# Kernel tuning notes

Hardware: AMD Instinct MI355X
Metric: run time of the kernel (lower is better)

## Reference

```python
import jax, jax.numpy as jnp
import numpy as np

CHANNEL = 8
K_DIM = 16
D = CHANNEL * K_DIM
ROUT_IT = 3
TAU = 1.0
EPS = 1e-12  # torch F.normalize default


def _normalize(v):
    # L2 normalize over last dim, matching torch.nn.functional.normalize
    nrm = jnp.sqrt(jnp.sum(v * v, axis=-1, keepdims=True))
    return v / jnp.maximum(nrm, EPS)


def setup_inputs() -> dict:
    key = jax.random.key(0)
    k1, k2, k3, k4 = jax.random.split(key, 4)
    n, m = 50000, 32
    in_dim = D  # in_caps * k_dim = 8*16
    x = jax.random.normal(k1, (n, in_dim), dtype=jnp.float32)
    stdv = 1.0 / np.sqrt(float(in_dim))
    W = jax.random.uniform(k2, (D, in_dim), dtype=jnp.float32, minval=-stdv, maxval=stdv)
    b = jax.random.uniform(k3, (D,), dtype=jnp.float32, minval=-stdv, maxval=stdv)
    neighbor_id = jax.random.randint(k4, (n * m,), 0, n + 1, dtype=jnp.int64)
    return {"x": x, "W": W, "b": b, "neighbor_id": neighbor_id}


def reference(x, W, b, neighbor_id):
    n = x.shape[0]
    m = neighbor_id.shape[0] // n
    # fc + relu
    x = jax.nn.relu(x @ W.T + b)
    # per-capsule normalize
    x = _normalize(x.reshape(n, CHANNEL, K_DIM)).reshape(n, D)
    # append zero row for padded neighbor ids, gather neighbors
    z = jnp.concatenate([x, jnp.zeros((1, D), dtype=x.dtype)], axis=0)
    neighbors = z[neighbor_id].reshape(n, m, CHANNEL, K_DIM)
    x_caps = x.reshape(n, CHANNEL, K_DIM)
    u = x_caps
    for it in range(ROUT_IT):
        # agreement logits per (node, neighbor, channel)
        p = jnp.einsum('nck,nmck->nmc', u, neighbors)
        p = jax.nn.softmax(p / TAU, axis=-1)  # softmax over channels
        u = jnp.einsum('nmc,nmck->nck', p, neighbors) + x_caps
        if it < ROUT_IT - 1:
            u = _normalize(u)
    return u.reshape(n, D)
```

## Files before the change

kernel.cpp:

```cpp
#include <hip/hip_runtime.h>
#include <math.h>

#define CHANNEL 8
#define KDIM 16
#define DFULL 128
#define MNBR 32
#define ROUT_IT 3
#define TM1 64
#define NBS 20
#define SLP 20

typedef __attribute__((ext_vector_type(4))) float f32x4;
typedef __attribute__((ext_vector_type(8))) short short8;
typedef __attribute__((ext_vector_type(8))) _Float16 half8;
typedef __attribute__((ext_vector_type(2))) _Float16 half2v;

__device__ inline unsigned pk16(float a, float b) {
  auto r = __builtin_amdgcn_cvt_pkrtz(a, b);
  return __builtin_bit_cast(unsigned, r);
}
__device__ inline float fdot2(unsigned a, unsigned b, float c) {
  return __builtin_amdgcn_fdot2(__builtin_bit_cast(half2v, a),
                                __builtin_bit_cast(half2v, b), c, false);
}
__device__ inline float h2f_bits(ushort s) {
  union { ushort u; _Float16 h; } v; v.u = s; return (float)v.h;
}
template <int C>
__device__ inline float dppadd(float x) {
  int m = __builtin_amdgcn_update_dpp(0, __builtin_bit_cast(int, x), C, 0xF, 0xF, true);
  return x + __builtin_bit_cast(float, m);
}
__device__ inline float dppswap1(float x) {
  int m = __builtin_amdgcn_update_dpp(0, __builtin_bit_cast(int, x), 0xB1, 0xF, 0xF, true);
  return __builtin_bit_cast(float, m);
}

union H8 { unsigned u[4]; short8 v; };
__device__ inline short8 pack8h(float4 a, float4 b) {
  H8 r;
  r.u[0] = pk16(a.x, a.y); r.u[1] = pk16(a.z, a.w);
  r.u[2] = pk16(b.x, b.y); r.u[3] = pk16(b.z, b.w);
  return r.v;
}

__global__ __launch_bounds__(256) void wpack_kernel(const float* __restrict__ W,
                                                    ushort* __restrict__ wpk) {
  int task = blockIdx.x * 256 + threadIdx.x;
  if (task >= 2048) return;
  int f = task >> 6, l = task & 63;
  int kk = f >> 3, j = f & 7, L = l & 15, H = l >> 4;
  const float* src = W + (size_t)(j * 16 + L) * 128 + kk * 32 + H * 8;
  float4 a = *(const float4*)src;
  float4 b = *(const float4*)(src + 4);
  *(short8*)(wpk + (size_t)task * 8) = pack8h(a, b);
}

__global__ __launch_bounds__(256) void fc_mfma_kernel(
    const float* __restrict__ x, const ushort* __restrict__ wpk,
    const float* __restrict__ bias, ushort* __restrict__ z16, int n) {
  __shared__ __align__(16) float smem[TM1 * 132];

  const int t = threadIdx.x, lane = t & 63, w = t >> 6;

  {
    const uint4* gw = (const uint4*)wpk;
    uint4* lw = (uint4*)smem;
#pragma unroll
    for (int i = 0; i < 8; ++i) lw[i * 256 + t] = gw[i * 256 + t];
  }

  const int L = lane & 15, H = lane >> 4;
  const int r0 = blockIdx.x * TM1;
  const int row = r0 + w * 16 + L;
  const bool ok = row < n;
  const float4 z4 = make_float4(0.f, 0.f, 0.f, 0.f);

  const float* xr = x + (size_t)row * DFULL + H * 8;
  short8 af[4];
#pragma unroll
  for (int kk = 0; kk < 4; ++kk) {
    float4 xa = ok ? *(const float4*)(xr + kk * 32) : z4;
    float4 xb = ok ? *(const float4*)(xr + kk * 32 + 4) : z4;
    af[kk] = pack8h(xa, xb);
  }

  f32x4 acc[8];
#pragma unroll
  for (int j = 0; j < 8; ++j) {
    float bv = bias[j * 16 + L];
    acc[j] = (f32x4){bv, bv, bv, bv};
  }
  __syncthreads();
  const short8* wf = (const short8*)smem;
#pragma unroll
  for (int j = 0; j < 8; ++j)
#pragma unroll
    for (int kk = 0; kk < 4; ++kk) {
      short8 bfr = wf[(kk * 8 + j) * 64 + lane];
      acc[j] = __builtin_amdgcn_mfma_f32_16x16x32_f16(
          __builtin_bit_cast(half8, af[kk]), __builtin_bit_cast(half8, bfr),
          acc[j], 0, 0, 0);
    }
  __syncthreads();

  float* ys = smem;
  const int lr = w * 16 + H * 4;
#pragma unroll
  for (int j = 0; j < 8; ++j)
#pragma unroll
    for (int r = 0; r < 4; ++r)
      ys[(lr + r) * 132 + j * 16 + L] = fmaxf(acc[j][r], 0.f);
  __syncthreads();

#pragma unroll
  for (int pass = 0; pass < 2; ++pass) {
    int task = t + pass * 256;
    int rr = task >> 3, cc = task & 7;
    const float4* yr = (const float4*)(ys + rr * 132 + cc * 16);
    float4 a = yr[0], b = yr[1], c4 = yr[2], d4 = yr[3];
    float ss = a.x * a.x;
    ss = fmaf(a.y, a.y, ss); ss = fmaf(a.z, a.z, ss); ss = fmaf(a.w, a.w, ss);
    ss = fmaf(b.x, b.x, ss); ss = fmaf(b.y, b.y, ss); ss = fmaf(b.z, b.z, ss);
    ss = fmaf(b.w, b.w, ss); ss = fmaf(c4.x, c4.x, ss); ss = fmaf(c4.y, c4.y, ss);
    ss = fmaf(c4.z, c4.z, ss); ss = fmaf(c4.w, c4.w, ss); ss = fmaf(d4.x, d4.x, ss);
    ss = fmaf(d4.y, d4.y, ss); ss = fmaf(d4.z, d4.z, ss); ss = fmaf(d4.w, d4.w, ss);
    float sc = 1.f / fmaxf(sqrtf(ss), 1e-12f);
    int grow = r0 + rr;
    if (grow < n) {
      uint4 o0, o1;
      o0.x = pk16(a.x * sc, a.y * sc);  o0.y = pk16(a.z * sc, a.w * sc);
      o0.z = pk16(b.x * sc, b.y * sc);  o0.w = pk16(b.z * sc, b.w * sc);
      o1.x = pk16(c4.x * sc, c4.y * sc); o1.y = pk16(c4.z * sc, c4.w * sc);
      o1.z = pk16(d4.x * sc, d4.y * sc); o1.w = pk16(d4.z * sc, d4.w * sc);
      uint4* dst = (uint4*)(z16 + (size_t)grow * DFULL + cc * 16);
      dst[0] = o0; dst[1] = o1;
    } else if (grow == n) {
      uint4 zz = {0u, 0u, 0u, 0u};
      uint4* dst = (uint4*)(z16 + (size_t)grow * DFULL + cc * 16);
      dst[0] = zz; dst[1] = zz;
    }
  }
}

__global__ __launch_bounds__(256) void routing_kernel(
    const ushort* __restrict__ z16, const int* __restrict__ nid,
    float* __restrict__ out, int n) {
  __shared__ __align__(16) unsigned nbT[2][DFULL * NBS];
  __shared__ __align__(16) unsigned slpk[2][CHANNEL * SLP];
  __shared__ __align__(16) unsigned ulpk[2][64];

  const int t = threadIdx.x;
  const int h = t >> 7, g = t & 127;
  const int node = 2 * blockIdx.x + h;
  const int p = g >> 3, c = g & 7;
  const int d = g, uc = g >> 4;

  int2 rp = *(const int2*)(nid + node * MNBR + 2 * p);
  const uint4* s0 = (const uint4*)(z16 + (size_t)rp.x * DFULL + c * KDIM);
  const uint4* s1 = (const uint4*)(z16 + (size_t)rp.y * DFULL + c * KDIM);
  uint4 Ra = s0[0], Rb = s0[1];
  uint4 Sa = s1[0], Sb = s1[1];

  unsigned aw[8] = {Ra.x, Ra.y, Ra.z, Ra.w, Rb.x, Rb.y, Rb.z, Rb.w};
  unsigned bw[8] = {Sa.x, Sa.y, Sa.z, Sa.w, Sb.x, Sb.y, Sb.z, Sb.w};
  {
    unsigned* nb = nbT[h];
    const int pc = (p + 4 * c) & 15;
#pragma unroll
    for (int i = 0; i < 8; ++i) {
      unsigned ev = __builtin_amdgcn_perm(bw[i], aw[i], 0x05040100u);
      unsigned od = __builtin_amdgcn_perm(bw[i], aw[i], 0x07060302u);
      nb[(c * KDIM + 2 * i) * NBS + pc] = ev;
      nb[(c * KDIM + 2 * i + 1) * NBS + pc] = od;
    }
  }
  unsigned xdw = *((const unsigned*)(z16 + (size_t)node * DFULL) + (d >> 1));
  const float xk = (d & 1) ? h2f_bits((ushort)(xdw >> 16))
                           : h2f_bits((ushort)(xdw & 0xffffu));
  if (!(d & 1)) ulpk[h][d >> 1] = xdw;
  __syncthreads();

  const unsigned* nr = nbT[h] + d * NBS;
  const uint4 n0 = *(const uint4*)(nr + 0);
  const uint4 n1 = *(const uint4*)(nr + 4);
  const uint4 n2 = *(const uint4*)(nr + 8);
  const uint4 n3 = *(const uint4*)(nr + 12);
  const uint4* sq0 = (const uint4*)(slpk[h] + uc * SLP + 4 * ((0 - uc) & 3));
  const uint4* sq1 = (const uint4*)(slpk[h] + uc * SLP + 4 * ((1 - uc) & 3));
  const uint4* sq2 = (const uint4*)(slpk[h] + uc * SLP + 4 * ((2 - uc) & 3));
  const uint4* sq3 = (const uint4*)(slpk[h] + uc * SLP + 4 * ((3 - uc) & 3));
  const uint4* up = (const uint4*)(ulpk[h] + c * 8);

  for (int it = 0; it < ROUT_IT; ++it) {
    {
      uint4 u0 = up[0], u1 = up[1];
      float A0 = 0.f, A1 = 0.f;
      A0 = fdot2(aw[0], u0.x, A0); A1 = fdot2(bw[0], u0.x, A1);
      A0 = fdot2(aw[1], u0.y, A0); A1 = fdot2(bw[1], u0.y, A1);
      A0 = fdot2(aw[2], u0.z, A0); A1 = fdot2(bw[2], u0.z, A1);
      A0 = fdot2(aw[3], u0.w, A0); A1 = fdot2(bw[3], u0.w, A1);
      A0 = fdot2(aw[4], u1.x, A0); A1 = fdot2(bw[4], u1.x, A1);
      A0 = fdot2(aw[5], u1.y, A0); A1 = fdot2(bw[5], u1.y, A1);
      A0 = fdot2(aw[6], u1.z, A0); A1 = fdot2(bw[6], u1.z, A1);
      A0 = fdot2(aw[7], u1.w, A0); A1 = fdot2(bw[7], u1.w, A1);
      float e0 = __expf(A0), e1 = __expf(A1);
      float d0 = dppadd<0xB1>(e0);  float d1 = dppadd<0xB1>(e1);
      d0 = dppadd<0x4E>(d0);        d1 = dppadd<0x4E>(d1);
      d0 = dppadd<0x141>(d0);       d1 = dppadd<0x141>(d1);
      float ir0 = __builtin_amdgcn_rcpf(d0);
      float ir1 = __builtin_amdgcn_rcpf(d1);
      slpk[h][c * SLP + p] = pk16(e0 * ir0, e1 * ir1);
    }
    __syncthreads();
    {
      uint4 v0 = *sq0, v1 = *sq1, v2 = *sq2, v3 = *sq3;
      float A0 = xk, A1 = 0.f;
      A0 = fdot2(n0.x, v0.x, A0); A1 = fdot2(n2.x, v2.x, A1);
      A0 = fdot2(n0.y, v0.y, A0); A1 = fdot2(n2.y, v2.y, A1);
      A0 = fdot2(n0.z, v0.z, A0); A1 = fdot2(n2.z, v2.z, A1);
      A0 = fdot2(n0.w, v0.w, A0); A1 = fdot2(n2.w, v2.w, A1);
      A0 = fdot2(n1.x, v1.x, A0); A1 = fdot2(n3.x, v3.x, A1);
      A0 = fdot2(n1.y, v1.y, A0); A1 = fdot2(n3.y, v3.y, A1);
      A0 = fdot2(n1.z, v1.z, A0); A1 = fdot2(n3.z, v3.z, A1);
      A0 = fdot2(n1.w, v1.w, A0); A1 = fdot2(n3.w, v3.w, A1);
      float u = A0 + A1;
      if (it == ROUT_IT - 1) {
        out[(size_t)node * DFULL + d] = u;
      } else {
        float ssq = u * u;
        ssq = dppadd<0xB1>(ssq);
        ssq = dppadd<0x4E>(ssq);
        ssq = dppadd<0x141>(ssq);
        ssq = dppadd<0x140>(ssq);
        float sc = 1.f / fmaxf(sqrtf(ssq), 1e-12f);
        float un = u * sc;
        float uo = dppswap1(un);
        if (!(d & 1)) ulpk[h][d >> 1] = pk16(un, uo);
      }
    }
    __syncthreads();
  }
}

extern "C" void kernel_launch(void* const* d_in, const int* in_sizes, int n_in,
                              void* d_out, int out_size, void* d_ws, size_t ws_size,
                              hipStream_t stream) {
  const float* x = (const float*)d_in[0];
  const float* W = (const float*)d_in[1];
  const float* b = (const float*)d_in[2];
  const int* nid = (const int*)d_in[3];
  float* out = (float*)d_out;

  int n = in_sizes[0] / DFULL;
  int g1 = (n + 1 + TM1 - 1) / TM1;
  size_t zrows = (size_t)g1 * TM1;

  ushort* z16 = (ushort*)d_ws;
  ushort* wpk = (ushort*)d_ws + zrows * DFULL;

  wpack_kernel<<<8, 256, 0, stream>>>(W, wpk);
  fc_mfma_kernel<<<g1, 256, 0, stream>>>(x, wpk, b, z16, n);
  routing_kernel<<<n / 2, 256, 0, stream>>>(z16, nid, out, n);
}
```

Before: 150.1 us.

## Map one node per wavefront in routing kernel, replacing barriers with LDS waits

```diff
diff --git a/kernel.cpp b/kernel.cpp
--- a/kernel.cpp
+++ b/kernel.cpp
@@ -8,7 +8,6 @@
 #define ROUT_IT 3
 #define TM1 64
 #define NBS 20
-#define SLP 20
 
 typedef __attribute__((ext_vector_type(4))) float f32x4;
 typedef __attribute__((ext_vector_type(8))) short short8;
@@ -23,8 +22,11 @@
   return __builtin_amdgcn_fdot2(__builtin_bit_cast(half2v, a),
                                 __builtin_bit_cast(half2v, b), c, false);
 }
-__device__ inline float h2f_bits(ushort s) {
-  union { ushort u; _Float16 h; } v; v.u = s; return (float)v.h;
+__device__ inline float h2f_lo(unsigned w) {
+  union { ushort u; _Float16 h; } v; v.u = (ushort)(w & 0xffffu); return (float)v.h;
+}
+__device__ inline float h2f_hi(unsigned w) {
+  union { ushort u; _Float16 h; } v; v.u = (ushort)(w >> 16); return (float)v.h;
 }
 template <int C>
 __device__ inline float dppadd(float x) {
@@ -143,103 +145,162 @@
   }
 }
 
-__global__ __launch_bounds__(256) void routing_kernel(
+__global__ __launch_bounds__(128, 3) void routing_kernel(
     const ushort* __restrict__ z16, const int* __restrict__ nid,
     float* __restrict__ out, int n) {
   __shared__ __align__(16) unsigned nbT[2][DFULL * NBS];
-  __shared__ __align__(16) unsigned slpk[2][CHANNEL * SLP];
-  __shared__ __align__(16) unsigned ulpk[2][64];
+  __shared__ __align__(16) unsigned slT[2][CHANNEL * NBS];
+  __shared__ __align__(16) unsigned ulk[2][64];
 
   const int t = threadIdx.x;
-  const int h = t >> 7, g = t & 127;
-  const int node = 2 * blockIdx.x + h;
-  const int p = g >> 3, c = g & 7;
-  const int d = g, uc = g >> 4;
-
-  int2 rp = *(const int2*)(nid + node * MNBR + 2 * p);
-  const uint4* s0 = (const uint4*)(z16 + (size_t)rp.x * DFULL + c * KDIM);
-  const uint4* s1 = (const uint4*)(z16 + (size_t)rp.y * DFULL + c * KDIM);
-  uint4 Ra = s0[0], Rb = s0[1];
-  uint4 Sa = s1[0], Sb = s1[1];
-
-  unsigned aw[8] = {Ra.x, Ra.y, Ra.z, Ra.w, Rb.x, Rb.y, Rb.z, Rb.w};
-  unsigned bw[8] = {Sa.x, Sa.y, Sa.z, Sa.w, Sb.x, Sb.y, Sb.z, Sb.w};
+  const int wv = t >> 6, lane = t & 63;
+  const int node = blockIdx.x * 2 + wv;
+  const int q = lane >> 3, c = lane & 7;
+  const int cu = lane >> 4;
+
+  int4 ids = *(const int4*)(nid + node * MNBR + 4 * q);
+  const uint4* g0 = (const uint4*)(z16 + (size_t)ids.x * DFULL + c * KDIM);
+  const uint4* g1 = (const uint4*)(z16 + (size_t)ids.y * DFULL + c * KDIM);
+  const uint4* g2 = (const uint4*)(z16 + (size_t)ids.z * DFULL + c * KDIM);
+  const uint4* g3 = (const uint4*)(z16 + (size_t)ids.w * DFULL + c * KDIM);
+  uint4 R0a = g0[0], R0b = g0[1];
+  uint4 R1a = g1[0], R1b = g1[1];
+  uint4 R2a = g2[0], R2b = g2[1];
+  uint4 R3a = g3[0], R3b = g3[1];
+
+  const unsigned* zdw = (const unsigned*)z16;
+  ulk[wv][lane] = zdw[(size_t)node * 64 + lane];
+  unsigned xw0 = zdw[(size_t)node * 64 + (lane >> 1)];
+  unsigned xw1 = zdw[(size_t)node * 64 + 32 + (lane >> 1)];
+  const float xk0 = (lane & 1) ? h2f_hi(xw0) : h2f_lo(xw0);
+  const float xk1 = (lane & 1) ? h2f_hi(xw1) : h2f_lo(xw1);
+
+  unsigned r0[8] = {R0a.x, R0a.y, R0a.z, R0a.w, R0b.x, R0b.y, R0b.z, R0b.w};
+  unsigned r1[8] = {R1a.x, R1a.y, R1a.z, R1a.w, R1b.x, R1b.y, R1b.z, R1b.w};
+  unsigned r2[8] = {R2a.x, R2a.y, R2a.z, R2a.w, R2b.x, R2b.y, R2b.z, R2b.w};
+  unsigned r3[8] = {R3a.x, R3a.y, R3a.z, R3a.w, R3b.x, R3b.y, R3b.z, R3b.w};
+
   {
-    unsigned* nb = nbT[h];
-    const int pc = (p + 4 * c) & 15;
+    unsigned* nb = nbT[wv];
+    const int sl0 = (2 * q + 4 * c) & 15;
+    const int sl1 = (2 * q + 1 + 4 * c) & 15;
 #pragma unroll
     for (int i = 0; i < 8; ++i) {
-      unsigned ev = __builtin_amdgcn_perm(bw[i], aw[i], 0x05040100u);
-      unsigned od = __builtin_amdgcn_perm(bw[i], aw[i], 0x07060302u);
-      nb[(c * KDIM + 2 * i) * NBS + pc] = ev;
-      nb[(c * KDIM + 2 * i + 1) * NBS + pc] = od;
-    }
-  }
-  unsigned xdw = *((const unsigned*)(z16 + (size_t)node * DFULL) + (d >> 1));
-  const float xk = (d & 1) ? h2f_bits((ushort)(xdw >> 16))
-                           : h2f_bits((ushort)(xdw & 0xffffu));
-  if (!(d & 1)) ulpk[h][d >> 1] = xdw;
-  __syncthreads();
-
-  const unsigned* nr = nbT[h] + d * NBS;
-  const uint4 n0 = *(const uint4*)(nr + 0);
-  const uint4 n1 = *(const uint4*)(nr + 4);
-  const uint4 n2 = *(const uint4*)(nr + 8);
-  const uint4 n3 = *(const uint4*)(nr + 12);
-  const uint4* sq0 = (const uint4*)(slpk[h] + uc * SLP + 4 * ((0 - uc) & 3));
-  const uint4* sq1 = (const uint4*)(slpk[h] + uc * SLP + 4 * ((1 - uc) & 3));
-  const uint4* sq2 = (const uint4*)(slpk[h] + uc * SLP + 4 * ((2 - uc) & 3));
-  const uint4* sq3 = (const uint4*)(slpk[h] + uc * SLP + 4 * ((3 - uc) & 3));
-  const uint4* up = (const uint4*)(ulpk[h] + c * 8);
-
+      unsigned ev0 = __builtin_amdgcn_perm(r1[i], r0[i], 0x05040100u);
+      unsigned od0 = __builtin_amdgcn_perm(r1[i], r0[i], 0x07060302u);
+      unsigned ev1 = __builtin_amdgcn_perm(r3[i], r2[i], 0x05040100u);
+      unsigned od1 = __builtin_amdgcn_perm(r3[i], r2[i], 0x07060302u);
+      nb[(c * KDIM + 2 * i) * NBS + sl0] = ev0;
+      nb[(c * KDIM + 2 * i + 1) * NBS + sl0] = od0;
+      nb[(c * KDIM + 2 * i) * NBS + sl1] = ev1;
+      nb[(c * KDIM + 2 * i + 1) * NBS + sl1] = od1;
+    }
+  }
+  asm volatile("s_waitcnt lgkmcnt(0)" ::: "memory");
+
+  const unsigned* colA = nbT[wv] + lane * NBS;
+  const unsigned* colB = nbT[wv] + (lane + 64) * NBS;
+  const uint4 nA0 = *(const uint4*)(colA + 0);
+  const uint4 nA1 = *(const uint4*)(colA + 4);
+  const uint4 nA2 = *(const uint4*)(colA + 8);
+  const uint4 nA3 = *(const uint4*)(colA + 12);
+  const uint4 nB0 = *(const uint4*)(colB + 0);
+  const uint4 nB1 = *(const uint4*)(colB + 4);
+  const uint4 nB2 = *(const uint4*)(colB + 8);
+  const uint4 nB3 = *(const uint4*)(colB + 12);
+
+  const uint4* upk = (const uint4*)(ulk[wv] + c * 8);
+  const int o0 = 4 * ((0 - cu) & 3), o1 = 4 * ((1 - cu) & 3),
+            o2 = 4 * ((2 - cu) & 3), o3 = 4 * ((3 - cu) & 3);
+  const unsigned* sA = slT[wv] + cu * NBS;
+  const unsigned* sB = slT[wv] + (cu + 4) * NBS;
+  uint2* swr = (uint2*)(slT[wv]) + c * (NBS / 2) + q;
+
+#pragma unroll
   for (int it = 0; it < ROUT_IT; ++it) {
     {
-      uint4 u0 = up[0], u1 = up[1];
-      float A0 = 0.f, A1 = 0.f;
-      A0 = fdot2(aw[0], u0.x, A0); A1 = fdot2(bw[0], u0.x, A1);
-      A0 = fdot2(aw[1], u0.y, A0); A1 = fdot2(bw[1], u0.y, A1);
-      A0 = fdot2(aw[2], u0.z, A0); A1 = fdot2(bw[2], u0.z, A1);
-      A0 = fdot2(aw[3], u0.w, A0); A1 = fdot2(bw[3], u0.w, A1);
-      A0 = fdot2(aw[4], u1.x, A0); A1 = fdot2(bw[4], u1.x, A1);
-      A0 = fdot2(aw[5], u1.y, A0); A1 = fdot2(bw[5], u1.y, A1);
-      A0 = fdot2(aw[6], u1.z, A0); A1 = fdot2(bw[6], u1.z, A1);
-      A0 = fdot2(aw[7], u1.w, A0); A1 = fdot2(bw[7], u1.w, A1);
-      float e0 = __expf(A0), e1 = __expf(A1);
-      float d0 = dppadd<0xB1>(e0);  float d1 = dppadd<0xB1>(e1);
-      d0 = dppadd<0x4E>(d0);        d1 = dppadd<0x4E>(d1);
-      d0 = dppadd<0x141>(d0);       d1 = dppadd<0x141>(d1);
-      float ir0 = __builtin_amdgcn_rcpf(d0);
-      float ir1 = __builtin_amdgcn_rcpf(d1);
-      slpk[h][c * SLP + p] = pk16(e0 * ir0, e1 * ir1);
-    }
-    __syncthreads();
+      uint4 ua = upk[0], ub = upk[1];
+      float A0 = 0.f, A1 = 0.f, A2 = 0.f, A3 = 0.f;
+      A0 = fdot2(r0[0], ua.x, A0); A1 = fdot2(r1[0], ua.x, A1);
+      A2 = fdot2(r2[0], ua.x, A2); A3 = fdot2(r3[0], ua.x, A3);
+      A0 = fdot2(r0[1], ua.y, A0); A1 = fdot2(r1[1], ua.y, A1);
+      A2 = fdot2(r2[1], ua.y, A2); A3 = fdot2(r3[1], ua.y, A3);
+      A0 = fdot2(r0[2], ua.z, A0); A1 = fdot2(r1[2], ua.z, A1);
+      A2 = fdot2(r2[2], ua.z, A2); A3 = fdot2(r3[2], ua.z, A3);
+      A0 = fdot2(r0[3], ua.w, A0); A1 = fdot2(r1[3], ua.w, A1);
+      A2 = fdot2(r2[3], ua.w, A2); A3 = fdot2(r3[3], ua.w, A3);
+      A0 = fdot2(r0[4], ub.x, A0); A1 = fdot2(r1[4], ub.x, A1);
+      A2 = fdot2(r2[4], ub.x, A2); A3 = fdot2(r3[4], ub.x, A3);
+      A0 = fdot2(r0[5], ub.y, A0); A1 = fdot2(r1[5], ub.y, A1);
+      A2 = fdot2(r2[5], ub.y, A2); A3 = fdot2(r3[5], ub.y, A3);
+      A0 = fdot2(r0[6], ub.z, A0); A1 = fdot2(r1[6], ub.z, A1);
+      A2 = fdot2(r2[6], ub.z, A2); A3 = fdot2(r3[6], ub.z, A3);
+      A0 = fdot2(r0[7], ub.w, A0); A1 = fdot2(r1[7], ub.w, A1);
+      A2 = fdot2(r2[7], ub.w, A2); A3 = fdot2(r3[7], ub.w, A3);
+      float e0 = __expf(A0), e1 = __expf(A1), e2 = __expf(A2), e3 = __expf(A3);
+      float D0 = dppadd<0x141>(dppadd<0x4E>(dppadd<0xB1>(e0)));
+      float D1 = dppadd<0x141>(dppadd<0x4E>(dppadd<0xB1>(e1)));
+      float D2 = dppadd<0x141>(dppadd<0x4E>(dppadd<0xB1>(e2)));
+      float D3 = dppadd<0x141>(dppadd<0x4E>(dppadd<0xB1>(e3)));
+      float s0 = e0 * __builtin_amdgcn_rcpf(D0);
+      float s1 = e1 * __builtin_amdgcn_rcpf(D1);
+      float s2 = e2 * __builtin_amdgcn_rcpf(D2);
+      float s3 = e3 * __builtin_amdgcn_rcpf(D3);
+      uint2 sw; sw.x = pk16(s0, s1); sw.y = pk16(s2, s3);
+      *swr = sw;
+    }
+    asm volatile("s_waitcnt lgkmcnt(0)" ::: "memory");
     {
-      uint4 v0 = *sq0, v1 = *sq1, v2 = *sq2, v3 = *sq3;
-      float A0 = xk, A1 = 0.f;
-      A0 = fdot2(n0.x, v0.x, A0); A1 = fdot2(n2.x, v2.x, A1);
-      A0 = fdot2(n0.y, v0.y, A0); A1 = fdot2(n2.y, v2.y, A1);
-      A0 = fdot2(n0.z, v0.z, A0); A1 = fdot2(n2.z, v2.z, A1);
-      A0 = fdot2(n0.w, v0.w, A0); A1 = fdot2(n2.w, v2.w, A1);
-      A0 = fdot2(n1.x, v1.x, A0); A1 = fdot2(n3.x, v3.x, A1);
-      A0 = fdot2(n1.y, v1.y, A0); A1 = fdot2(n3.y, v3.y, A1);
-      A0 = fdot2(n1.z, v1.z, A0); A1 = fdot2(n3.z, v3.z, A1);
-      A0 = fdot2(n1.w, v1.w, A0); A1 = fdot2(n3.w, v3.w, A1);
-      float u = A0 + A1;
+      uint4 v;
+      float a = xk0, b = 0.f;
+      v = *(const uint4*)(sA + o0);
+      a = fdot2(nA0.x, v.x, a); b = fdot2(nA0.y, v.y, b);
+      a = fdot2(nA0.z, v.z, a); b = fdot2(nA0.w, v.w, b);
+      v = *(const uint4*)(sA + o1);
+      a = fdot2(nA1.x, v.x, a); b = fdot2(nA1.y, v.y, b);
+      a = fdot2(nA1.z, v.z, a); b = fdot2(nA1.w, v.w, b);
+      v = *(const uint4*)(sA + o2);
+      a = fdot2(nA2.x, v.x, a); b = fdot2(nA2.y, v.y, b);
+      a = fdot2(nA2.z, v.z, a); b = fdot2(nA2.w, v.w, b);
+      v = *(const uint4*)(sA + o3);
+      a = fdot2(nA3.x, v.x, a); b = fdot2(nA3.y, v.y, b);
+      a = fdot2(nA3.z, v.z, a); b = fdot2(nA3.w, v.w, b);
+      float u0 = a + b;
+      float e = xk1, f = 0.f;
+      v = *(const uint4*)(sB + o0);
+      e = fdot2(nB0.x, v.x, e); f = fdot2(nB0.y, v.y, f);
+      e = fdot2(nB0.z, v.z, e); f = fdot2(nB0.w, v.w, f);
+      v = *(const uint4*)(sB + o1);
+      e = fdot2(nB1.x, v.x, e); f = fdot2(nB1.y, v.y, f);
+      e = fdot2(nB1.z, v.z, e); f = fdot2(nB1.w, v.w, f);
+      v = *(const uint4*)(sB + o2);
+      e = fdot2(nB2.x, v.x, e); f = fdot2(nB2.y, v.y, f);
+      e = fdot2(nB2.z, v.z, e); f = fdot2(nB2.w, v.w, f);
+      v = *(const uint4*)(sB + o3);
+      e = fdot2(nB3.x, v.x, e); f = fdot2(nB3.y, v.y, f);
+      e = fdot2(nB3.z, v.z, e); f = fdot2(nB3.w, v.w, f);
+      float u1 = e + f;
       if (it == ROUT_IT - 1) {
-        out[(size_t)node * DFULL + d] = u;
+        out[(size_t)node * DFULL + lane] = u0;
+        out[(size_t)node * DFULL + 64 + lane] = u1;
       } else {
-        float ssq = u * u;
-        ssq = dppadd<0xB1>(ssq);
-        ssq = dppadd<0x4E>(ssq);
-        ssq = dppadd<0x141>(ssq);
-        ssq = dppadd<0x140>(ssq);
-        float sc = 1.f / fmaxf(sqrtf(ssq), 1e-12f);
-        float un = u * sc;
-        float uo = dppswap1(un);
-        if (!(d & 1)) ulpk[h][d >> 1] = pk16(un, uo);
+        float ss0 = u0 * u0;
+        ss0 = dppadd<0xB1>(ss0); ss0 = dppadd<0x4E>(ss0);
+        ss0 = dppadd<0x141>(ss0); ss0 = dppadd<0x140>(ss0);
+        float ss1 = u1 * u1;
+        ss1 = dppadd<0xB1>(ss1); ss1 = dppadd<0x4E>(ss1);
+        ss1 = dppadd<0x141>(ss1); ss1 = dppadd<0x140>(ss1);
+        float sc0 = __builtin_amdgcn_rsqf(fmaxf(ss0, 1e-24f));
+        float sc1 = __builtin_amdgcn_rsqf(fmaxf(ss1, 1e-24f));
+        float un0 = u0 * sc0, un1 = u1 * sc1;
+        float p0 = dppswap1(un0), p1 = dppswap1(un1);
+        if (!(lane & 1)) {
+          ulk[wv][lane >> 1] = pk16(un0, p0);
+          ulk[wv][32 + (lane >> 1)] = pk16(un1, p1);
+        }
       }
     }
-    __syncthreads();
+    asm volatile("s_waitcnt lgkmcnt(0)" ::: "memory");
   }
 }
 
@@ -261,5 +322,5 @@
 
   wpack_kernel<<<8, 256, 0, stream>>>(W, wpk);
   fc_mfma_kernel<<<g1, 256, 0, stream>>>(x, wpk, b, z16, n);
-  routing_kernel<<<n / 2, 256, 0, stream>>>(z16, nid, out, n);
-}
+  routing_kernel<<<n / 2, 128, 0, stream>>>(z16, nid, out, n);
+}
```

Result: no change. 149.6 us (-0.4%).
